# Optimization experiments

Measured on AMD Instinct MI355X. Metric: run time of the kernel, lower is better.

Reference implementation:

```python
import jax, jax.numpy as jnp
import numpy as np

B, T, E, NH, VOCAB, MULT = 1, 1024, 768, 12, 32000, 32
N = E * MULT // NH  # 2048
LN_EPS = 1e-5


def setup_inputs() -> dict:
    key = jax.random.key(0)
    ks = jax.random.split(key, 6)
    return {
        "idx": jax.random.randint(ks[0], (B, T), 0, VOCAB),
        "embed": jax.random.normal(ks[1], (VOCAB, E), jnp.float32) * 0.02,
        "encoder": jax.random.normal(ks[2], (NH, E, N), jnp.float32) * 0.02,
        "encoder_v": jax.random.normal(ks[3], (NH, E, N), jnp.float32) * 0.02,
        "decoder": jax.random.normal(ks[4], (NH * N, E), jnp.float32) * 0.02,
        "lm_head": jax.random.normal(ks[5], (VOCAB, E), jnp.float32) * 0.02,
        "ln_w": jnp.ones((E,), jnp.float32),
        "ln_b": jnp.zeros((E,), jnp.float32),
        "n_layer": 6,
    }


def reference(idx, embed, encoder, encoder_v, decoder, lm_head, ln_w, ln_b, n_layer):
    nh, e, n = encoder.shape
    t = idx.shape[1]
    dec = decoder.reshape(nh, n, e)  # flatten order (h, n) -> h*N + n

    def ln(x):
        m = jnp.mean(x, axis=-1, keepdims=True)
        v = jnp.mean(jnp.square(x - m), axis=-1, keepdims=True)
        return (x - m) * jax.lax.rsqrt(v + LN_EPS) * ln_w + ln_b

    causal = jnp.tril(jnp.ones((t, t), bool))  # [T, T]
    scale = 1.0 / np.sqrt(n).astype(np.float32)

    x = ln(embed[idx])  # [B, T, E]  (the unsqueezed head dim broadcasts; keep it squeezed)
    for _ in range(n_layer):
        # encoder projection + ReLU: [B,T,E] x [H,E,N] -> [B,H,T,N]
        x_sparse = jax.nn.relu(jnp.einsum("bte,hen->bhtn", x, encoder))
        # hand-rolled causal attention, Q=K=x_sparse, V=x (broadcast over heads)
        scores = jnp.einsum("bhqn,bhkn->bhqk", x_sparse, x_sparse) * scale
        scores = jnp.where(causal, scores, -jnp.inf)
        attn = jax.nn.softmax(scores, axis=-1)
        y = jnp.einsum("bhqk,bke->bhqe", attn, x)  # [B,H,T,E]
        y = ln(y)
        y_sparse = jax.nn.relu(jnp.einsum("bhte,hen->bhtn", y, encoder_v))
        xy = x_sparse * y_sparse  # [B,H,T,N]; dropout p=0 -> identity
        y_mlp = jnp.einsum("bhtn,hne->bte", xy, dec)  # decoder matmul
        x = ln(x + ln(y_mlp))
    logits = jnp.einsum("bte,ve->btv", x, lm_head)
    return logits
```

## Files before the change

### kernel.cpp

```cpp
#include <hip/hip_runtime.h>

typedef unsigned short u16;
typedef short bf16x8 __attribute__((ext_vector_type(8)));
typedef float f32x4 __attribute__((ext_vector_type(4)));
typedef u16 u16x4 __attribute__((ext_vector_type(4)));

#define TT     1024
#define EE     768
#define NHH    12
#define ND     2048
#define VOC    32000
#define HNN    24576
#define NLAYER 6
#define LN_EPS 1e-5f
#define SPLITK 16

__device__ __forceinline__ float b2f(u16 u){
  unsigned int x = ((unsigned int)u) << 16; float f; __builtin_memcpy(&f, &x, 4); return f;
}
__device__ __forceinline__ u16 f2b(float f){
  unsigned int x; __builtin_memcpy(&x, &f, 4);
  x = x + 0x7fffu + ((x >> 16) & 1u);
  return (u16)(x >> 16);
}

__device__ __forceinline__ void gload16(const void* g, void* lds){
  __builtin_amdgcn_global_load_lds(
      (const __attribute__((address_space(1))) unsigned int*)g,
      (__attribute__((address_space(3))) unsigned int*)(unsigned int)(unsigned long long)lds,
      16, 0, 0);
}

__device__ __forceinline__ bf16x8 ldsr(unsigned addr){
  bf16x8 r;
  asm volatile("ds_read_b128 %0, %1" : "=v"(r) : "v"(addr));
  return r;
}

__device__ __forceinline__ void blk_sum2(float& a, float& b){
  #pragma unroll
  for (int o = 32; o > 0; o >>= 1){ a += __shfl_down(a, o); b += __shfl_down(b, o); }
  __shared__ float sa[4], sb[4];
  int lane = threadIdx.x & 63, wid = threadIdx.x >> 6;
  __syncthreads();
  if (lane == 0){ sa[wid] = a; sb[wid] = b; }
  __syncthreads();
  a = (sa[0] + sa[1]) + (sa[2] + sa[3]);
  b = (sb[0] + sb[1]) + (sb[2] + sb[3]);
}
__device__ __forceinline__ float blk_max(float v){
  #pragma unroll
  for (int o = 32; o > 0; o >>= 1) v = fmaxf(v, __shfl_down(v, o));
  __shared__ float sm[4];
  int lane = threadIdx.x & 63, wid = threadIdx.x >> 6;
  __syncthreads();
  if (lane == 0) sm[wid] = v;
  __syncthreads();
  return fmaxf(fmaxf(sm[0], sm[1]), fmaxf(sm[2], sm[3]));
}
__device__ __forceinline__ float blk_sum(float v){
  #pragma unroll
  for (int o = 32; o > 0; o >>= 1) v += __shfl_down(v, o);
  __shared__ float ss[4];
  int lane = threadIdx.x & 63, wid = threadIdx.x >> 6;
  __syncthreads();
  if (lane == 0) ss[wid] = v;
  __syncthreads();
  return (ss[0] + ss[1]) + (ss[2] + ss[3]);
}

__global__ void transpose_f2b(const float* __restrict__ in, long sIn,
                              u16* __restrict__ out, long sOut, int R, int Cc){
  __shared__ float tile[32][33];
  int z = blockIdx.z;
  in  += (long)z * sIn;
  out += (long)z * sOut;
  int c0 = blockIdx.x * 32, r0 = blockIdx.y * 32;
  int lx = threadIdx.x & 31, ly = threadIdx.x >> 5;
  #pragma unroll
  for (int i = 0; i < 32; i += 8)
    tile[ly + i][lx] = in[(long)(r0 + ly + i) * Cc + (c0 + lx)];
  __syncthreads();
  #pragma unroll
  for (int i = 0; i < 32; i += 8)
    out[(long)(c0 + ly + i) * R + (r0 + lx)] = f2b(tile[lx][ly + i]);
}

__global__ void conv_f2b(const float* __restrict__ in, u16* __restrict__ out){
  long i = ((long)blockIdx.x * 256 + threadIdx.x) * 4;
  float4 v = *(const float4*)(in + i);
  u16x4 o; o.x = f2b(v.x); o.y = f2b(v.y); o.z = f2b(v.z); o.w = f2b(v.w);
  *(u16x4*)(out + i) = o;
}

__global__ void embed_ln(const int* __restrict__ idx, const float* __restrict__ emb,
                         const float* __restrict__ w, const float* __restrict__ b,
                         float* __restrict__ xf, u16* __restrict__ xb, u16* __restrict__ xT){
  int t = blockIdx.x, tid = threadIdx.x;
  const float* src = emb + (long)idx[t] * EE;
  float v[3];
  #pragma unroll
  for (int j = 0; j < 3; j++) v[j] = src[tid + j * 256];
  float s = v[0] + v[1] + v[2];
  float s2 = v[0]*v[0] + v[1]*v[1] + v[2]*v[2];
  blk_sum2(s, s2);
  float m  = s * (1.0f / EE);
  float var = s2 * (1.0f / EE) - m * m;
  float rs = rsqrtf(var + LN_EPS);
  #pragma unroll
  for (int j = 0; j < 3; j++){
    int e = tid + j * 256;
    float o = (v[j] - m) * rs * w[e] + b[e];
    xf[(long)t * EE + e] = o;
    u16 ob = f2b(o);
    xb[(long)t * EE + e] = ob;
    xT[(long)e * TT + t] = ob;
  }
}

__global__ void ln_rows(const float* __restrict__ in, u16* __restrict__ out,
                        const float* __restrict__ w, const float* __restrict__ b){
  long row = blockIdx.x; int tid = threadIdx.x;
  const float* src = in + row * EE;
  float v[3];
  #pragma unroll
  for (int j = 0; j < 3; j++) v[j] = src[tid + j * 256];
  float s = v[0] + v[1] + v[2];
  float s2 = v[0]*v[0] + v[1]*v[1] + v[2]*v[2];
  blk_sum2(s, s2);
  float m = s * (1.0f / EE);
  float var = s2 * (1.0f / EE) - m * m;
  float rs = rsqrtf(var + LN_EPS);
  #pragma unroll
  for (int j = 0; j < 3; j++){
    int e = tid + j * 256;
    out[row * EE + e] = f2b((v[j] - m) * rs * w[e] + b[e]);
  }
}

__global__ void softmax_rows(const float* __restrict__ scores, u16* __restrict__ attn){
  int q = blockIdx.x, h = blockIdx.y, tid = threadIdx.x;
  const float* srow = scores + ((long)h * TT + q) * TT;
  u16* arow = attn + ((long)h * TT + q) * TT;
  float4 v = *(const float4*)(srow + tid * 4);
  float mx = blk_max(fmaxf(fmaxf(v.x, v.y), fmaxf(v.z, v.w)));
  float e0 = __expf(v.x - mx), e1 = __expf(v.y - mx);
  float e2 = __expf(v.z - mx), e3 = __expf(v.w - mx);
  float inv = 1.0f / blk_sum(e0 + e1 + e2 + e3);
  u16x4 o; o.x = f2b(e0 * inv); o.y = f2b(e1 * inv); o.z = f2b(e2 * inv); o.w = f2b(e3 * inv);
  *(u16x4*)(arow + tid * 4) = o;
}

template<int P>
__global__ void residual_ln(const float* __restrict__ part, const float* __restrict__ xin,
                            float* __restrict__ xf, u16* __restrict__ xb, u16* __restrict__ xT,
                            const float* __restrict__ w, const float* __restrict__ b){
  int t = blockIdx.x, tid = threadIdx.x;
  float g[3];
  #pragma unroll
  for (int j = 0; j < 3; j++){
    int e = tid + j * 256;
    float s = 0.f;
    #pragma unroll
    for (int pp = 0; pp < P; pp++) s += part[((long)pp * TT + t) * EE + e];
    g[j] = s;
  }
  float s = g[0] + g[1] + g[2], s2 = g[0]*g[0] + g[1]*g[1] + g[2]*g[2];
  blk_sum2(s, s2);
  float m = s * (1.0f / EE), var = s2 * (1.0f / EE) - m * m;
  float rs = rsqrtf(var + LN_EPS);
  float hh[3];
  #pragma unroll
  for (int j = 0; j < 3; j++){
    int e = tid + j * 256;
    hh[j] = xin[(long)t * EE + e] + ((g[j] - m) * rs * w[e] + b[e]);
  }
  s = hh[0] + hh[1] + hh[2]; s2 = hh[0]*hh[0] + hh[1]*hh[1] + hh[2]*hh[2];
  blk_sum2(s, s2);
  m = s * (1.0f / EE); var = s2 * (1.0f / EE) - m * m; rs = rsqrtf(var + LN_EPS);
  #pragma unroll
  for (int j = 0; j < 3; j++){
    int e = tid + j * 256;
    float o = (hh[j] - m) * rs * w[e] + b[e];
    xf[(long)t * EE + e] = o;
    u16 ob = f2b(o);
    xb[(long)t * EE + e] = ob;
    xT[(long)e * TT + t] = ob;
  }
}

template<int EPI>
__global__ __launch_bounds__(512, 2)
void g8(const u16* __restrict__ Ab, long sA,
        const u16* __restrict__ Bb, long sB,
        void* __restrict__ Cb, long sC,
        int grid_m, int grid_mn,
        int K, int lda, int ldb, int ldc, float scale,
        const u16* __restrict__ Mul, long sMul, int ldmul){
  __shared__ __align__(16) u16 S[69632];

  const int nwg = gridDim.x, orig = blockIdx.x;
  const int q = nwg >> 3, r = nwg & 7, xcd = orig & 7;
  const int wgid = (xcd < r ? xcd*(q+1) : r*(q+1) + (xcd - r)*q) + (orig >> 3);
  const int z   = wgid / grid_mn;
  const int rem = wgid - z*grid_mn;
  const int nb  = rem / grid_m;
  const int mb  = rem - nb*grid_m;
  const int m0 = mb*256, n0 = nb*256;
  const int tid = threadIdx.x, lane = tid & 63, wid = tid >> 6;

  if (EPI == 2 && n0 > m0 + 255){
    float* C = (float*)Cb + (long)z * sC;
    #pragma unroll
    for (int i = 0; i < 32; i++){
      int idx4 = (tid + i*512)*4;
      int rr = idx4 >> 8, cc = idx4 & 255;
      *(float4*)&C[(long)(m0+rr)*ldc + n0 + cc] = make_float4(-1e30f,-1e30f,-1e30f,-1e30f);
    }
    return;
  }

  const u16* A = Ab + (long)z*sA;
  const u16* B = Bb + (long)z*sB;

  const int rS = wid*16 + (lane >> 2);
  const int cS = (((lane & 3) ^ ((rS >> 1) & 3)) << 3);
  const u16* gA = A + (long)(m0 + rS)*lda + cS;
  const u16* gB = B + (long)(n0 + rS)*ldb + cS;

  char* Sb = (char*)&S[0];
  const unsigned db0 = 0, db1 = 65536u, scr = 131072u;
  auto issue = [&](const u16* src, unsigned dstOff){
    gload16(src, Sb + dstOff + (unsigned)wid*1024u);
  };

  const int wr = wid >> 2, wc = wid & 3;
  const int fr = lane & 15, fk = lane >> 4;
  const unsigned base = (unsigned)(unsigned long long)Sb;
  unsigned aOff[8], bOff[4];
  #pragma unroll
  for (int mi = 0; mi < 8; mi++){
    int row = wr*128 + mi*16 + fr;
    aOff[mi] = (unsigned)(row*64 + ((fk ^ ((row >> 1) & 3)) << 4));
  }
  #pragma unroll
  for (int ni = 0; ni < 4; ni++){
    int row = wc*64 + ni*16 + fr;
    bOff[ni] = 32768u + (unsigned)(row*64 + ((fk ^ ((row >> 1) & 3)) << 4));
  }

  const int NT = K >> 6;
  const long lda128 = (long)128*lda, ldb128 = (long)128*ldb;

  f32x4 acc[8][4] = {};

  issue(gA,              db0);          issue(gA + lda128,          db0 + 8192u);
  issue(gB,              db0+32768u);   issue(gB + ldb128,          db0 + 40960u);
  issue(gA + 32,         db0+16384u);   issue(gA + 32 + lda128,     db0 + 24576u);
  issue(gB + 32,         db0+49152u);   issue(gB + 32 + ldb128,     db0 + 57344u);
  issue(gA + 64,         db1);          issue(gA + 64 + lda128,     db1 + 8192u);
  issue(gB + 64,         db1+32768u);   issue(gB + 64 + ldb128,     db1 + 40960u);
  asm volatile("s_waitcnt vmcnt(8)" ::: "memory");
  __builtin_amdgcn_s_barrier();
  __builtin_amdgcn_sched_barrier(0);

  for (int t = 0; t < NT; t++){
    const unsigned cur = (t & 1) ? db1 : db0;
    const unsigned oth = (t & 1) ? db0 : db1;
    const bool v1 = (t + 1 < NT), v2 = (t + 2 < NT);
    const long k1 = (long)(v1 ? t + 1 : 0) * 64;
    const long k2 = (long)(v2 ? t + 2 : 0) * 64;
    const unsigned d1A = v1 ? oth + 16384u : scr;
    const unsigned d1B = v1 ? oth + 49152u : scr;
    const unsigned d2A = v2 ? cur           : scr;
    const unsigned d2B = v2 ? cur + 32768u  : scr;
    bf16x8 a[4], b[4];

    #pragma unroll
    for (int ni = 0; ni < 4; ni++) b[ni] = ldsr(base + cur + bOff[ni]);
    #pragma unroll
    for (int u = 0; u < 4; u++)    a[u]  = ldsr(base + cur + aOff[u]);
    issue(gA + k1 + 32, d1A); issue(gA + k1 + 32 + lda128, d1A + 8192u);
    __builtin_amdgcn_s_barrier();
    asm volatile("s_waitcnt lgkmcnt(0)" ::: "memory");
    __builtin_amdgcn_sched_barrier(0);
    __builtin_amdgcn_s_setprio(1);
    #pragma unroll
    for (int u = 0; u < 4; u++)
      #pragma unroll
      for (int ni = 0; ni < 4; ni++)
        acc[u][ni] = __builtin_amdgcn_mfma_f32_16x16x32_bf16(a[u], b[ni], acc[u][ni], 0, 0, 0);
    __builtin_amdgcn_s_setprio(0);
    __builtin_amdgcn_s_barrier();
    __builtin_amdgcn_sched_barrier(0);

    #pragma unroll
    for (int u = 0; u < 4; u++) a[u] = ldsr(base + cur + aOff[4 + u]);
    issue(gB + k1 + 32, d1B); issue(gB + k1 + 32 + ldb128, d1B + 8192u);
    __builtin_amdgcn_s_barrier();
    asm volatile("s_waitcnt lgkmcnt(0)" ::: "memory");
    __builtin_amdgcn_sched_barrier(0);
    __builtin_amdgcn_s_setprio(1);
    #pragma unroll
    for (int u = 0; u < 4; u++)
      #pragma unroll
      for (int ni = 0; ni < 4; ni++)
        acc[4+u][ni] = __builtin_amdgcn_mfma_f32_16x16x32_bf16(a[u], b[ni], acc[4+u][ni], 0, 0, 0);
    __builtin_amdgcn_s_setprio(0);
    asm volatile("s_waitcnt vmcnt(8)" ::: "memory");
    __builtin_amdgcn_s_barrier();
    __builtin_amdgcn_sched_barrier(0);

    #pragma unroll
    for (int ni = 0; ni < 4; ni++) b[ni] = ldsr(base + cur + bOff[ni] + 16384u);
    #pragma unroll
    for (int u = 0; u < 4; u++)    a[u]  = ldsr(base + cur + aOff[u] + 16384u);
    issue(gA + k2, d2A); issue(gA + k2 + lda128, d2A + 8192u);
    __builtin_amdgcn_s_barrier();
    asm volatile("s_waitcnt lgkmcnt(0)" ::: "memory");
    __builtin_amdgcn_sched_barrier(0);
    __builtin_amdgcn_s_setprio(1);
    #pragma unroll
    for (int u = 0; u < 4; u++)
      #pragma unroll
      for (int ni = 0; ni < 4; ni++)
        acc[u][ni] = __builtin_amdgcn_mfma_f32_16x16x32_bf16(a[u], b[ni], acc[u][ni], 0, 0, 0);
    __builtin_amdgcn_s_setprio(0);
    __builtin_amdgcn_s_barrier();
    __builtin_amdgcn_sched_barrier(0);

    #pragma unroll
    for (int u = 0; u < 4; u++) a[u] = ldsr(base + cur + aOff[4 + u] + 16384u);
    issue(gB + k2, d2B); issue(gB + k2 + ldb128, d2B + 8192u);
    __builtin_amdgcn_s_barrier();
    asm volatile("s_waitcnt lgkmcnt(0)" ::: "memory");
    __builtin_amdgcn_sched_barrier(0);
    __builtin_amdgcn_s_setprio(1);
    #pragma unroll
    for (int u = 0; u < 4; u++)
      #pragma unroll
      for (int ni = 0; ni < 4; ni++)
        acc[4+u][ni] = __builtin_amdgcn_mfma_f32_16x16x32_bf16(a[u], b[ni], acc[4+u][ni], 0, 0, 0);
    __builtin_amdgcn_s_setprio(0);
    asm volatile("s_waitcnt vmcnt(8)" ::: "memory");
    __builtin_amdgcn_s_barrier();
    __builtin_amdgcn_sched_barrier(0);
  }
  asm volatile("s_waitcnt vmcnt(0)" ::: "memory");

  const int er = (lane >> 4) * 4, ec = lane & 15;
  #pragma unroll
  for (int mi = 0; mi < 8; mi++){
    #pragma unroll
    for (int ni = 0; ni < 4; ni++){
      #pragma unroll
      for (int j = 0; j < 4; j++){
        int row = m0 + wr*128 + mi*16 + er + j;
        int col = n0 + wc*64 + ni*16 + ec;
        float v = acc[mi][ni][j];
        if (EPI == 0){
          ((float*)Cb + (long)z * sC)[(long)row * ldc + col] = v;
        } else if (EPI == 1){
          v = v > 0.f ? v : 0.f;
          ((u16*)Cb + (long)z * sC)[(long)row * ldc + col] = f2b(v);
        } else if (EPI == 2){
          v *= scale;
          if (col > row) v = -1e30f;
          ((float*)Cb + (long)z * sC)[(long)row * ldc + col] = v;
        } else {
          v = v > 0.f ? v : 0.f;
          float mfv = b2f((Mul + (long)z * sMul)[(long)row * ldmul + col]);
          ((u16*)Cb + (long)z * sC)[(long)row * ldc + col] = f2b(v * mfv);
        }
      }
    }
  }
}

template<int EPI, bool CCLAMP>
__global__ __launch_bounds__(256, 2)
void gemmw(const u16* __restrict__ Ab, long sA,
           const u16* __restrict__ Bb, long sB,
           void* __restrict__ Cb, long sC,
           int grid_m, int grid_mn,
           int K, int lda, int ldb, int ldc, float scale,
           const u16* __restrict__ Mul, long sMul, int ldmul){
  constexpr unsigned BUFB = 24576u;
  __shared__ __align__(16) u16 S[3 * 12288];

  const int nwg = gridDim.x, orig = blockIdx.x;
  const int q = nwg >> 3, r = nwg & 7, xcd = orig & 7;
  const int wgid = (xcd < r ? xcd*(q+1) : r*(q+1) + (xcd - r)*q) + (orig >> 3);
  const int z   = wgid / grid_mn;
  const int rem = wgid - z*grid_mn;
  const int nb  = rem / grid_m;
  const int mb  = rem - nb*grid_m;
  const int m0 = mb*128, n0 = nb*256;
  const int tid = threadIdx.x, lane = tid & 63, wid = tid >> 6;

  if (EPI == 2 && n0 > m0 + 127){
    float* C = (float*)Cb + (long)z * sC;
    #pragma unroll
    for (int i = 0; i < 32; i++){
      int idx4 = (tid + i*256)*4;
      int rr = idx4 >> 8, cc = idx4 & 255;
      *(float4*)&C[(long)(m0+rr)*ldc + n0 + cc] = make_float4(-1e30f,-1e30f,-1e30f,-1e30f);
    }
    return;
  }

  const u16* A = Ab + (long)z*sA;
  const u16* B = Bb + (long)z*sB;

  const int rS = tid >> 2;
  const int cS = (((tid & 3) ^ ((rS >> 1) & 3)) << 3);
  const u16* gA[2]; const u16* gB[4];
  #pragma unroll
  for (int i = 0; i < 2; i++) gA[i] = A + (long)(m0 + i*64 + rS)*lda + cS;
  #pragma unroll
  for (int i = 0; i < 4; i++) gB[i] = B + (long)(n0 + i*64 + rS)*ldb + cS;

  char* Sb = (char*)&S[0];
  auto stage = [&](int kt, unsigned bB){
    const int ko = kt << 5;
    gload16(gA[0] + ko, Sb + bB +          wid*1024u);
    gload16(gA[1] + ko, Sb + bB +  4096u + wid*1024u);
    #pragma unroll
    for (int i = 0; i < 4; i++)
      gload16(gB[i] + ko, Sb + bB + 8192u + i*4096u + wid*1024u);
  };

  const int wr = wid >> 1, wc = wid & 1;
  const int fr = lane & 15, fk = lane >> 4;
  const unsigned base = (unsigned)(unsigned long long)Sb;
  unsigned aAd[4], bAd[8];
  #pragma unroll
  for (int mi = 0; mi < 4; mi++){
    int row = wr*64 + mi*16 + fr;
    aAd[mi] = base + (unsigned)(row*64 + ((fk ^ ((row >> 1) & 3)) << 4));
  }
  #pragma unroll
  for (int ni = 0; ni < 8; ni++){
    int row = wc*128 + ni*16 + fr;
    bAd[ni] = base + 8192u + (unsigned)(row*64 + ((fk ^ ((row >> 1) & 3)) << 4));
  }

  const int Keff = CCLAMP ? (m0 + 128 < K ? m0 + 128 : K) : K;
  const int NT = Keff >> 5;
  const int s0 = (mb*13 + nb*7 + z*5) % NT;

  f32x4 acc[4][8] = {};

  int p1 = s0 + 1; if (p1 >= NT) p1 -= NT;
  stage(s0, 0);
  stage(p1, BUFB);
  asm volatile("s_waitcnt vmcnt(6)" ::: "memory");
  __builtin_amdgcn_s_barrier();
  __builtin_amdgcn_sched_barrier(0);

  unsigned rbB = 0, wbB = 2u*BUFB;
  for (int t = 0; t < NT; t++){
    int nx = (t + 2 < NT) ? t + 2 : NT - 1;
    int ph = s0 + nx; if (ph >= NT) ph -= NT;
    stage(ph, wbB);
    bf16x8 afr[4], bfr[8];
    #pragma unroll
    for (int ni = 0; ni < 8; ni++) bfr[ni] = ldsr(bAd[ni] + rbB);
    #pragma unroll
    for (int mi = 0; mi < 4; mi++) afr[mi] = ldsr(aAd[mi] + rbB);
    __builtin_amdgcn_s_barrier();
    asm volatile("s_waitcnt lgkmcnt(0)" ::: "memory");
    __builtin_amdgcn_sched_barrier(0);
    __builtin_amdgcn_s_setprio(1);
    #pragma unroll
    for (int mi = 0; mi < 4; mi++)
      #pragma unroll
      for (int ni = 0; ni < 8; ni++)
        acc[mi][ni] = __builtin_amdgcn_mfma_f32_16x16x32_bf16(afr[mi], bfr[ni], acc[mi][ni], 0, 0, 0);
    __builtin_amdgcn_s_setprio(0);
    __builtin_amdgcn_sched_barrier(0);
    asm volatile("s_waitcnt vmcnt(6)" ::: "memory");
    __builtin_amdgcn_s_barrier();
    __builtin_amdgcn_sched_barrier(0);
    unsigned tmp = rbB; rbB += BUFB; if (rbB == 3u*BUFB) rbB = 0;
    wbB = tmp;
  }
  asm volatile("s_waitcnt vmcnt(0)" ::: "memory");

  const int er = (lane >> 4) * 4, ec = lane & 15;
  #pragma unroll
  for (int mi = 0; mi < 4; mi++){
    #pragma unroll
    for (int ni = 0; ni < 8; ni++){
      #pragma unroll
      for (int j = 0; j < 4; j++){
        int row = m0 + wr*64 + mi*16 + er + j;
        int col = n0 + wc*128 + ni*16 + ec;
        float v = acc[mi][ni][j];
        if (EPI == 0){
          ((float*)Cb + (long)z * sC)[(long)row * ldc + col] = v;
        } else if (EPI == 1){
          v = v > 0.f ? v : 0.f;
          ((u16*)Cb + (long)z * sC)[(long)row * ldc + col] = f2b(v);
        } else if (EPI == 2){
          v *= scale;
          if (col > row) v = -1e30f;
          ((float*)Cb + (long)z * sC)[(long)row * ldc + col] = v;
        } else {
          v = v > 0.f ? v : 0.f;
          float mfv = b2f((Mul + (long)z * sMul)[(long)row * ldmul + col]);
          ((u16*)Cb + (long)z * sC)[(long)row * ldc + col] = f2b(v * mfv);
        }
      }
    }
  }
}

extern "C" void kernel_launch(void* const* d_in, const int* in_sizes, int n_in,
                              void* d_out, int out_size, void* d_ws, size_t ws_size,
                              hipStream_t stream){
  (void)in_sizes; (void)n_in; (void)out_size; (void)ws_size;
  const int*   idx     = (const int*)  d_in[0];
  const float* embed   = (const float*)d_in[1];
  const float* encoder = (const float*)d_in[2];
  const float* encv    = (const float*)d_in[3];
  const float* decoder = (const float*)d_in[4];
  const float* lm_head = (const float*)d_in[5];
  const float* ln_w    = (const float*)d_in[6];
  const float* ln_b    = (const float*)d_in[7];
  float* out = (float*)d_out;

  char* p = (char*)d_ws;
  auto take = [&](size_t n){ char* r = p; p += (n + 255) & ~(size_t)255; return r; };
  u16*   encT  = (u16*)  take((size_t)NHH * ND * EE * 2);
  u16*   encvT = (u16*)  take((size_t)NHH * ND * EE * 2);
  u16*   decT  = (u16*)  take((size_t)EE * HNN * 2);
  u16*   lmhB  = (u16*)  take((size_t)VOC * EE * 2);
  float* xf    = (float*)take((size_t)TT * EE * 4);
  u16*   xb    = (u16*)  take((size_t)TT * EE * 2);
  u16*   xT    = (u16*)  take((size_t)EE * TT * 2);
  u16*   xs    = (u16*)  take((size_t)NHH * TT * ND * 2);
  char*  big   =         take((size_t)NHH * TT * TT * 4);
  u16*   attn  = (u16*)  take((size_t)NHH * TT * TT * 2);
  u16*   yb    = (u16*)  take((size_t)NHH * TT * EE * 2);
  take((size_t)8 * TT * EE * 4);
  float* scores = (float*)big;
  float* yf     = (float*)big;
  u16*   xy     = (u16*)big;
  float* part   = (float*)attn;

  dim3 blk(256, 1, 1);

  transpose_f2b<<<dim3(ND / 32, EE / 32, NHH), blk, 0, stream>>>(encoder, (long)EE * ND, encT,  (long)ND * EE, EE, ND);
  transpose_f2b<<<dim3(ND / 32, EE / 32, NHH), blk, 0, stream>>>(encv,    (long)EE * ND, encvT, (long)ND * EE, EE, ND);
  transpose_f2b<<<dim3(EE / 32, HNN / 32, 1),  blk, 0, stream>>>(decoder, 0, decT, 0, HNN, EE);
  conv_f2b<<<dim3((VOC * EE) / 1024, 1, 1), blk, 0, stream>>>(lm_head, lmhB);

  embed_ln<<<dim3(TT, 1, 1), blk, 0, stream>>>(idx, embed, ln_w, ln_b, xf, xb, xT);

  const float scl = 0.022097086912079608f;

  for (int L = 0; L < NLAYER; ++L){
    g8<1><<<dim3(4*8*NHH), dim3(512), 0, stream>>>(
        xb, 0, encT, (long)ND * EE, xs, (long)TT * ND,
        4, 32, EE, EE, EE, ND, 0.f, (const u16*)0, 0, 0);
    g8<2><<<dim3(4*4*NHH), dim3(512), 0, stream>>>(
        xs, (long)TT * ND, xs, (long)TT * ND, scores, (long)TT * TT,
        4, 16, ND, ND, ND, TT, scl, (const u16*)0, 0, 0);
    softmax_rows<<<dim3(TT, NHH, 1), blk, 0, stream>>>(scores, attn);
    gemmw<0,true><<<dim3(8*3*NHH), blk, 0, stream>>>(
        attn, (long)TT * TT, xT, 0, yf, (long)TT * EE,
        8, 24, TT, TT, TT, EE, 0.f, (const u16*)0, 0, 0);
    ln_rows<<<dim3(NHH * TT, 1, 1), blk, 0, stream>>>(yf, yb, ln_w, ln_b);
    g8<3><<<dim3(4*8*NHH), dim3(512), 0, stream>>>(
        yb, (long)TT * EE, encvT, (long)ND * EE, xy, (long)ND,
        4, 32, EE, EE, EE, HNN, 0.f, xs, (long)TT * ND, ND);
    gemmw<0,false><<<dim3(8*3*SPLITK), blk, 0, stream>>>(
        xy, (long)(HNN / SPLITK), decT, (long)(HNN / SPLITK), part, (long)TT * EE,
        8, 24, HNN / SPLITK, HNN, HNN, EE, 0.f, (const u16*)0, 0, 0);
    residual_ln<SPLITK><<<dim3(TT, 1, 1), blk, 0, stream>>>(part, xf, xf, xb, xT, ln_w, ln_b);
  }

  g8<0><<<dim3(4*125), dim3(512), 0, stream>>>(
      xb, 0, lmhB, 0, out, 0,
      4, 500, EE, EE, EE, VOC, 0.f, (const u16*)0, 0, 0);
}
```

Before: 1.992 ms.

## Skip masked score tiles, causal-aware softmax, and bf16 split-K partials

The scores GEMM no longer writes -1e30 fill for fully masked tiles and drops the per-element causal mask. Instead the softmax reads only the first q+1 entries of each row and writes zeros up to a 128-aligned pad, which cuts traffic on the scores and attention buffers. The decoder split-K partials are now stored as bf16 instead of fp32, halving partial-sum traffic, and unused epilogue variants of the wide GEMM are removed. The trade-offs are lower precision in the 16-way partial sum and a reliance on the attention GEMM's causal clamp never reading attention entries past the padded length.

New measurement: 1.964 ms. Within noise of the previous version (-1.4%).

```diff
diff --git a/kernel.cpp b/kernel.cpp
--- a/kernel.cpp
+++ b/kernel.cpp
@@ -142,17 +142,36 @@
   int q = blockIdx.x, h = blockIdx.y, tid = threadIdx.x;
   const float* srow = scores + ((long)h * TT + q) * TT;
   u16* arow = attn + ((long)h * TT + q) * TT;
-  float4 v = *(const float4*)(srow + tid * 4);
-  float mx = blk_max(fmaxf(fmaxf(v.x, v.y), fmaxf(v.z, v.w)));
-  float e0 = __expf(v.x - mx), e1 = __expf(v.y - mx);
-  float e2 = __expf(v.z - mx), e3 = __expf(v.w - mx);
-  float inv = 1.0f / blk_sum(e0 + e1 + e2 + e3);
-  u16x4 o; o.x = f2b(e0 * inv); o.y = f2b(e1 * inv); o.z = f2b(e2 * inv); o.w = f2b(e3 * inv);
-  *(u16x4*)(arow + tid * 4) = o;
+  const int len = q + 1;
+  const int pad = (q + 128) & ~127;
+  float v[4];
+  float mx = -1e30f;
+  #pragma unroll
+  for (int j = 0; j < 4; j++){
+    int i = tid + j * 256;
+    if (i < len){ v[j] = srow[i]; mx = fmaxf(mx, v[j]); }
+  }
+  mx = blk_max(mx);
+  float s = 0.f;
+  #pragma unroll
+  for (int j = 0; j < 4; j++){
+    int i = tid + j * 256;
+    if (i < len){ v[j] = __expf(v[j] - mx); s += v[j]; }
+  }
+  float inv = 1.0f / blk_sum(s);
+  #pragma unroll
+  for (int j = 0; j < 4; j++){
+    int i = tid + j * 256;
+    if (i < pad){
+      u16 o = 0;
+      if (i < len) o = f2b(v[j] * inv);
+      arow[i] = o;
+    }
+  }
 }
 
 template<int P>
-__global__ void residual_ln(const float* __restrict__ part, const float* __restrict__ xin,
+__global__ void residual_ln(const u16* __restrict__ part, const float* __restrict__ xin,
                             float* __restrict__ xf, u16* __restrict__ xb, u16* __restrict__ xT,
                             const float* __restrict__ w, const float* __restrict__ b){
   int t = blockIdx.x, tid = threadIdx.x;
@@ -162,7 +181,7 @@
     int e = tid + j * 256;
     float s = 0.f;
     #pragma unroll
-    for (int pp = 0; pp < P; pp++) s += part[((long)pp * TT + t) * EE + e];
+    for (int pp = 0; pp < P; pp++) s += b2f(part[((long)pp * TT + t) * EE + e]);
     g[j] = s;
   }
   float s = g[0] + g[1] + g[2], s2 = g[0]*g[0] + g[1]*g[1] + g[2]*g[2];
@@ -209,16 +228,7 @@
   const int m0 = mb*256, n0 = nb*256;
   const int tid = threadIdx.x, lane = tid & 63, wid = tid >> 6;
 
-  if (EPI == 2 && n0 > m0 + 255){
-    float* C = (float*)Cb + (long)z * sC;
-    #pragma unroll
-    for (int i = 0; i < 32; i++){
-      int idx4 = (tid + i*512)*4;
-      int rr = idx4 >> 8, cc = idx4 & 255;
-      *(float4*)&C[(long)(m0+rr)*ldc + n0 + cc] = make_float4(-1e30f,-1e30f,-1e30f,-1e30f);
-    }
-    return;
-  }
+  if (EPI == 2 && n0 > m0 + 255) return;
 
   const u16* A = Ab + (long)z*sA;
   const u16* B = Bb + (long)z*sB;
@@ -364,9 +374,7 @@
           v = v > 0.f ? v : 0.f;
           ((u16*)Cb + (long)z * sC)[(long)row * ldc + col] = f2b(v);
         } else if (EPI == 2){
-          v *= scale;
-          if (col > row) v = -1e30f;
-          ((float*)Cb + (long)z * sC)[(long)row * ldc + col] = v;
+          ((float*)Cb + (long)z * sC)[(long)row * ldc + col] = v * scale;
         } else {
           v = v > 0.f ? v : 0.f;
           float mfv = b2f((Mul + (long)z * sMul)[(long)row * ldmul + col]);
@@ -383,8 +391,7 @@
            const u16* __restrict__ Bb, long sB,
            void* __restrict__ Cb, long sC,
            int grid_m, int grid_mn,
-           int K, int lda, int ldb, int ldc, float scale,
-           const u16* __restrict__ Mul, long sMul, int ldmul){
+           int K, int lda, int ldb, int ldc){
   constexpr unsigned BUFB = 24576u;
   __shared__ __align__(16) u16 S[3 * 12288];
 
@@ -398,17 +405,6 @@
   const int m0 = mb*128, n0 = nb*256;
   const int tid = threadIdx.x, lane = tid & 63, wid = tid >> 6;
 
-  if (EPI == 2 && n0 > m0 + 127){
-    float* C = (float*)Cb + (long)z * sC;
-    #pragma unroll
-    for (int i = 0; i < 32; i++){
-      int idx4 = (tid + i*256)*4;
-      int rr = idx4 >> 8, cc = idx4 & 255;
-      *(float4*)&C[(long)(m0+rr)*ldc + n0 + cc] = make_float4(-1e30f,-1e30f,-1e30f,-1e30f);
-    }
-    return;
-  }
-
   const u16* A = Ab + (long)z*sA;
   const u16* B = Bb + (long)z*sB;
 
@@ -499,17 +495,8 @@
         float v = acc[mi][ni][j];
         if (EPI == 0){
           ((float*)Cb + (long)z * sC)[(long)row * ldc + col] = v;
-        } else if (EPI == 1){
-          v = v > 0.f ? v : 0.f;
+        } else {
           ((u16*)Cb + (long)z * sC)[(long)row * ldc + col] = f2b(v);
-        } else if (EPI == 2){
-          v *= scale;
-          if (col > row) v = -1e30f;
-          ((float*)Cb + (long)z * sC)[(long)row * ldc + col] = v;
-        } else {
-          v = v > 0.f ? v : 0.f;
-          float mfv = b2f((Mul + (long)z * sMul)[(long)row * ldmul + col]);
-          ((u16*)Cb + (long)z * sC)[(long)row * ldc + col] = f2b(v * mfv);
         }
       }
     }
@@ -547,7 +534,7 @@
   float* scores = (float*)big;
   float* yf     = (float*)big;
   u16*   xy     = (u16*)big;
-  float* part   = (float*)attn;
+  u16*   part   = attn;
 
   dim3 blk(256, 1, 1);
 
@@ -570,14 +557,14 @@
     softmax_rows<<<dim3(TT, NHH, 1), blk, 0, stream>>>(scores, attn);
     gemmw<0,true><<<dim3(8*3*NHH), blk, 0, stream>>>(
         attn, (long)TT * TT, xT, 0, yf, (long)TT * EE,
-        8, 24, TT, TT, TT, EE, 0.f, (const u16*)0, 0, 0);
+        8, 24, TT, TT, TT, EE);
     ln_rows<<<dim3(NHH * TT, 1, 1), blk, 0, stream>>>(yf, yb, ln_w, ln_b);
     g8<3><<<dim3(4*8*NHH), dim3(512), 0, stream>>>(
         yb, (long)TT * EE, encvT, (long)ND * EE, xy, (long)ND,
         4, 32, EE, EE, EE, HNN, 0.f, xs, (long)TT * ND, ND);
-    gemmw<0,false><<<dim3(8*3*SPLITK), blk, 0, stream>>>(
+    gemmw<4,false><<<dim3(8*3*SPLITK), blk, 0, stream>>>(
         xy, (long)(HNN / SPLITK), decT, (long)(HNN / SPLITK), part, (long)TT * EE,
-        8, 24, HNN / SPLITK, HNN, HNN, EE, 0.f, (const u16*)0, 0, 0);
+        8, 24, HNN / SPLITK, HNN, HNN, EE);
     residual_ln<SPLITK><<<dim3(TT, 1, 1), blk, 0, stream>>>(part, xf, xf, xb, xT, ln_w, ln_b);
   }
 
```
